# Kernel tuning notes

Hardware: AMD Instinct MI355X
Metric: run time of the kernel (lower is better)

The kernel has to match this reference:

```python
import jax, jax.numpy as jnp
import numpy as np

EMBED_DIM = 1024
NUM_HEADS = 16
HEAD_DIM = EMBED_DIM // NUM_HEADS
B, NQ, K = 2, 2048, 2048


def setup_inputs() -> dict:
    key = jax.random.key(0)
    ks = jax.random.split(key, 11)
    s = 1.0 / np.sqrt(EMBED_DIM)
    return {
        "Q_input": jax.random.normal(ks[0], (B, NQ, EMBED_DIM), jnp.float32),
        "K_input": jax.random.normal(ks[1], (B, K, EMBED_DIM), jnp.float32),
        "V_input": jax.random.normal(ks[2], (B, K, EMBED_DIM), jnp.float32),
        "Wq": jax.random.normal(ks[3], (EMBED_DIM, EMBED_DIM), jnp.float32) * s,
        "bq": jnp.zeros((EMBED_DIM,), jnp.float32),
        "Wk": jax.random.normal(ks[4], (EMBED_DIM, EMBED_DIM), jnp.float32) * s,
        "bk": jnp.zeros((EMBED_DIM,), jnp.float32),
        "Wv": jax.random.normal(ks[5], (EMBED_DIM, EMBED_DIM), jnp.float32) * s,
        "bv": jnp.zeros((EMBED_DIM,), jnp.float32),
        "Wo": jax.random.normal(ks[6], (EMBED_DIM, EMBED_DIM), jnp.float32) * s,
        "bo": jnp.zeros((EMBED_DIM,), jnp.float32),
    }


def reference(Q_input, K_input, V_input, Wq, bq, Wk, bk, Wv, bv, Wo, bo):
    b, n_q, _ = Q_input.shape
    k = K_input.shape[1]
    # Linear projections (torch Linear: x @ W.T + b)
    Q = Q_input @ Wq.T + bq
    Kp = K_input @ Wk.T + bk
    V = V_input @ Wv.T + bv
    # [b, h, s, d]
    Q = Q.reshape(b, n_q, NUM_HEADS, HEAD_DIM).transpose(0, 2, 1, 3)
    Kp = Kp.reshape(b, k, NUM_HEADS, HEAD_DIM).transpose(0, 2, 1, 3)
    V = V.reshape(b, k, NUM_HEADS, HEAD_DIM).transpose(0, 2, 1, 3)
    scores = jnp.einsum("bhqd,bhkd->bhqk", Q, Kp) / jnp.sqrt(jnp.float32(HEAD_DIM))
    weights = jax.nn.softmax(scores, axis=-1)
    attn = jnp.einsum("bhqk,bhkd->bhqd", weights, V)
    attn = attn.transpose(0, 2, 1, 3).reshape(b, n_q, EMBED_DIM)
    return attn @ Wo.T + bo
```

## Files before the change

kernel.cpp:

```cpp
#include <hip/hip_runtime.h>
#include <hip/hip_bf16.h>

typedef __bf16  bf16x8 __attribute__((ext_vector_type(8)));
typedef float   f32x4  __attribute__((ext_vector_type(4)));

#define EMB   1024
#define QSTR  3072
#define HD    64
#define NH    16
#define SEQ   2048
#define BATCH 2
#define TOKENS (BATCH*SEQ)
#define TK    64

typedef __attribute__((address_space(1))) unsigned int* gp_t;
typedef __attribute__((address_space(3))) unsigned int* lp_t;
__device__ __forceinline__ void gload16(const __bf16* g, __bf16* l) {
    __builtin_amdgcn_global_load_lds((gp_t)(unsigned long long)(const void*)g,
                                     (lp_t)(unsigned int)(unsigned long long)(void*)l,
                                     16, 0, 0);
}

__global__ __launch_bounds__(256) void cvt4_kernel(
    const float* __restrict__ s0, const float* __restrict__ s1,
    const float* __restrict__ s2, const float* __restrict__ s3,
    __bf16* __restrict__ dst, int n_per)
{
    const float* s = (blockIdx.y == 0) ? s0 : (blockIdx.y == 1) ? s1
                   : (blockIdx.y == 2) ? s2 : s3;
    int i = (blockIdx.x * 256 + threadIdx.x) * 8;
    if (i >= n_per) return;
    float4 a = *(const float4*)(s + i);
    float4 b = *(const float4*)(s + i + 4);
    __bf16 o[8] = {(__bf16)a.x, (__bf16)a.y, (__bf16)a.z, (__bf16)a.w,
                   (__bf16)b.x, (__bf16)b.y, (__bf16)b.z, (__bf16)b.w};
    *(uint4*)(dst + (size_t)blockIdx.y * n_per + i) = *(const uint4*)o;
}

template <typename TY>
__global__ __launch_bounds__(256) void gemm_fast(
    const __bf16* __restrict__ X, const __bf16* __restrict__ Wt,
    const float* __restrict__ b0, const float* __restrict__ b1,
    const float* __restrict__ b2, TY* __restrict__ Y, int ldy)
{
    __shared__ __align__(16) __bf16 As[2][128 * 64];
    __shared__ __align__(16) __bf16 Bs[2][64 * 64];

    const int tid  = threadIdx.x;
    const int wave = tid >> 6;
    const int lane = tid & 63;
    const int quad = lane >> 4;
    const int l16  = lane & 15;
    const int warp_m = wave >> 1;
    const int warp_n = wave & 1;

    const int bm = blockIdx.y;
    const int bn = blockIdx.x;

    const int lr = lane >> 3;
    const int lc = (lane & 7) ^ lr;
    const __bf16* Ag = X + (size_t)(bn >> 4) * TOKENS * EMB
                         + (size_t)(bm * 128 + wave * 32 + lr) * EMB + lc * 8;
    const __bf16* Bg = Wt + (size_t)(bn * 64 + wave * 16 + lr) * EMB + lc * 8;
    const int aoff = wave * 2048;
    const int boff = wave * 1024;

    f32x4 acc[4][2] = {};

    gload16(Ag,            As[0] + aoff);
    gload16(Ag +  8 * EMB, As[0] + aoff + 512);
    gload16(Ag + 16 * EMB, As[0] + aoff + 1024);
    gload16(Ag + 24 * EMB, As[0] + aoff + 1536);
    gload16(Bg,            Bs[0] + boff);
    gload16(Bg +  8 * EMB, Bs[0] + boff + 512);

    for (int t = 0; t < EMB / 64; ++t) {
        const int cur = t & 1, nxt = cur ^ 1;
        __syncthreads();
        if (t + 1 < EMB / 64) {
            const __bf16* a0 = Ag + (t + 1) * 64;
            const __bf16* w0 = Bg + (t + 1) * 64;
            gload16(a0,            As[nxt] + aoff);
            gload16(a0 +  8 * EMB, As[nxt] + aoff + 512);
            gload16(a0 + 16 * EMB, As[nxt] + aoff + 1024);
            gload16(a0 + 24 * EMB, As[nxt] + aoff + 1536);
            gload16(w0,            Bs[nxt] + boff);
            gload16(w0 +  8 * EMB, Bs[nxt] + boff + 512);
        }

        #pragma unroll
        for (int kk = 0; kk < 2; ++kk) {
            bf16x8 af[4], bf[2];
            #pragma unroll
            for (int i = 0; i < 4; ++i) {
                int row = warp_m * 64 + i * 16 + l16;
                af[i] = *(const bf16x8*)(As[cur] + (row * 8 + ((kk * 4 + quad) ^ (row & 7))) * 8);
            }
            #pragma unroll
            for (int j = 0; j < 2; ++j) {
                int row = warp_n * 32 + j * 16 + l16;
                bf[j] = *(const bf16x8*)(Bs[cur] + (row * 8 + ((kk * 4 + quad) ^ (row & 7))) * 8);
            }
            #pragma unroll
            for (int i = 0; i < 4; ++i)
                #pragma unroll
                for (int j = 0; j < 2; ++j)
                    acc[i][j] = __builtin_amdgcn_mfma_f32_16x16x32_bf16(af[i], bf[j], acc[i][j], 0, 0, 0);
        }
    }

    #pragma unroll
    for (int i = 0; i < 4; ++i)
        #pragma unroll
        for (int j = 0; j < 2; ++j) {
            int n = bn * 64 + warp_n * 32 + j * 16 + l16;
            const float* bsel = (n < 1024) ? b0 : (n < 2048) ? b1 : b2;
            float bj = bsel[n & 1023];
            #pragma unroll
            for (int r = 0; r < 4; ++r) {
                int m = bm * 128 + warp_m * 64 + i * 16 + quad * 4 + r;
                Y[(size_t)m * ldy + n] = (TY)(acc[i][j][r] + bj);
            }
        }
}

__global__ __launch_bounds__(256) void attn_kernel(
    const __bf16* __restrict__ QKV, __bf16* __restrict__ Op)
{
    __shared__ __bf16 Ks[2][64][72];
    __shared__ __bf16 Vt[2][64][72];
    __shared__ __bf16 Plds[4][16][72];

    const int tid  = threadIdx.x;
    const int wave = tid >> 6;
    const int lane = tid & 63;
    const int quad = lane >> 4;
    const int l16  = lane & 15;

    const int qt = blockIdx.x;
    const int h  = blockIdx.y;
    const int b  = blockIdx.z;

    const size_t qoff  = (size_t)b * SEQ * QSTR + (size_t)h * HD;
    const size_t obase = (size_t)b * SEQ * EMB  + (size_t)h * HD;
    const int qbase = qt * 64 + wave * 16;

    const __bf16* qrow = QKV + qoff + (size_t)(qbase + l16) * QSTR;
    bf16x8 aq0 = *(const bf16x8*)(qrow +      quad * 8);
    bf16x8 aq1 = *(const bf16x8*)(qrow + 32 + quad * 8);
    #pragma unroll
    for (int i = 0; i < 8; ++i) {
        aq0[i] = (__bf16)((float)aq0[i] * 0.125f);
        aq1[i] = (__bf16)((float)aq1[i] * 0.125f);
    }

    float l_run[4] = {0.f, 0.f, 0.f, 0.f};
    f32x4 oacc[4] = {};

    const __bf16* Kg = QKV + qoff + EMB;
    const __bf16* Vg = QKV + qoff + 2 * EMB;

    const int srow = tid >> 3;
    const int scol = (tid & 7) << 3;
    const int g0 = srow >> 3;
    const int g1 = g0 + 4;

    {
        uint4 k0 = *(const uint4*)(Kg + (size_t)(srow     ) * QSTR + scol);
        uint4 k1 = *(const uint4*)(Kg + (size_t)(srow + 32) * QSTR + scol);
        uint4 v0 = *(const uint4*)(Vg + (size_t)(srow     ) * QSTR + scol);
        uint4 v1 = *(const uint4*)(Vg + (size_t)(srow + 32) * QSTR + scol);
        *(uint4*)&Ks[0][srow     ][scol] = k0;
        *(uint4*)&Ks[0][srow + 32][scol] = k1;
        const __bf16* p0 = (const __bf16*)&v0;
        const __bf16* p1 = (const __bf16*)&v1;
        #pragma unroll
        for (int j = 0; j < 8; ++j) {
            int d  = scol + j;
            int gg = (d >> 3) & 7;
            Vt[0][d][((g0 ^ gg) << 3) + (srow & 7)] = p0[j];
            Vt[0][d][((g1 ^ gg) << 3) + (srow & 7)] = p1[j];
        }
    }
    __syncthreads();

    for (int t = 0; t < SEQ / TK; ++t) {
        const int cur = t & 1, nxt = cur ^ 1;
        const bool have_next = (t + 1) < SEQ / TK;
        uint4 nk0, nk1, nv0, nv1;
        if (have_next) {
            int kb = (t + 1) * TK;
            nk0 = *(const uint4*)(Kg + (size_t)(kb + srow     ) * QSTR + scol);
            nk1 = *(const uint4*)(Kg + (size_t)(kb + srow + 32) * QSTR + scol);
            nv0 = *(const uint4*)(Vg + (size_t)(kb + srow     ) * QSTR + scol);
            nv1 = *(const uint4*)(Vg + (size_t)(kb + srow + 32) * QSTR + scol);
        }

        f32x4 s[4] = {};
        #pragma unroll
        for (int kb16 = 0; kb16 < 4; ++kb16) {
            bf16x8 klo = *(const bf16x8*)&Ks[cur][kb16 * 16 + l16][     quad * 8];
            bf16x8 khi = *(const bf16x8*)&Ks[cur][kb16 * 16 + l16][32 + quad * 8];
            s[kb16] = __builtin_amdgcn_mfma_f32_16x16x32_bf16(aq0, klo, s[kb16], 0, 0, 0);
            s[kb16] = __builtin_amdgcn_mfma_f32_16x16x32_bf16(aq1, khi, s[kb16], 0, 0, 0);
        }

        #pragma unroll
        for (int kb16 = 0; kb16 < 4; ++kb16)
            #pragma unroll
            for (int r = 0; r < 4; ++r) {
                float e = __expf(s[kb16][r]);
                s[kb16][r] = e;
                l_run[r] += e;
            }

        #pragma unroll
        for (int kb16 = 0; kb16 < 4; ++kb16)
            #pragma unroll
            for (int r = 0; r < 4; ++r)
                Plds[wave][quad * 4 + r][kb16 * 16 + l16] = (__bf16)s[kb16][r];
        __builtin_amdgcn_fence(__ATOMIC_ACQ_REL, "workgroup");

        bf16x8 ap0 = *(const bf16x8*)&Plds[wave][l16][     quad * 8];
        bf16x8 ap1 = *(const bf16x8*)&Plds[wave][l16][32 + quad * 8];
        #pragma unroll
        for (int dt = 0; dt < 4; ++dt) {
            int d  = dt * 16 + l16;
            int gg = (d >> 3) & 7;
            bf16x8 bv0 = *(const bf16x8*)&Vt[cur][d][(( quad     ^ gg) << 3)];
            bf16x8 bv1 = *(const bf16x8*)&Vt[cur][d][(((quad + 4) ^ gg) << 3)];
            oacc[dt] = __builtin_amdgcn_mfma_f32_16x16x32_bf16(ap0, bv0, oacc[dt], 0, 0, 0);
            oacc[dt] = __builtin_amdgcn_mfma_f32_16x16x32_bf16(ap1, bv1, oacc[dt], 0, 0, 0);
        }

        if (have_next) {
            *(uint4*)&Ks[nxt][srow     ][scol] = nk0;
            *(uint4*)&Ks[nxt][srow + 32][scol] = nk1;
            const __bf16* p0 = (const __bf16*)&nv0;
            const __bf16* p1 = (const __bf16*)&nv1;
            #pragma unroll
            for (int j = 0; j < 8; ++j) {
                int d  = scol + j;
                int gg = (d >> 3) & 7;
                Vt[nxt][d][((g0 ^ gg) << 3) + (srow & 7)] = p0[j];
                Vt[nxt][d][((g1 ^ gg) << 3) + (srow & 7)] = p1[j];
            }
        }
        __syncthreads();
    }

    #pragma unroll
    for (int off = 1; off < 16; off <<= 1)
        #pragma unroll
        for (int r = 0; r < 4; ++r)
            l_run[r] += __shfl_xor(l_run[r], off, 64);

    #pragma unroll
    for (int dt = 0; dt < 4; ++dt)
        #pragma unroll
        for (int r = 0; r < 4; ++r) {
            int q = qbase + quad * 4 + r;
            float v = oacc[dt][r] / l_run[r];
            Op[obase + (size_t)q * EMB + dt * 16 + l16] = (__bf16)v;
        }
}

extern "C" void kernel_launch(void* const* d_in, const int* in_sizes, int n_in,
                              void* d_out, int out_size, void* d_ws, size_t ws_size,
                              hipStream_t stream) {
    const float* Qin = (const float*)d_in[0];
    const float* Kin = (const float*)d_in[1];
    const float* Vin = (const float*)d_in[2];
    const float* Wq  = (const float*)d_in[3];
    const float* bq  = (const float*)d_in[4];
    const float* Wk  = (const float*)d_in[5];
    const float* bk  = (const float*)d_in[6];
    const float* Wv  = (const float*)d_in[7];
    const float* bv  = (const float*)d_in[8];
    const float* Wo  = (const float*)d_in[9];
    const float* bo  = (const float*)d_in[10];

    const size_t TENS = (size_t)TOKENS * EMB;
    const size_t WEL  = (size_t)EMB * EMB;
    __bf16* ws = (__bf16*)d_ws;
    __bf16* Xin  = ws;
    __bf16* Wb   = ws + 3 * TENS;
    __bf16* QKVp = ws + 3 * TENS + 4 * WEL;
    __bf16* Ap   = ws;

    cvt4_kernel<<<dim3((unsigned)(TENS / 2048), 3), 256, 0, stream>>>(
        Qin, Kin, Vin, Vin, Xin, (int)TENS);
    cvt4_kernel<<<dim3((unsigned)(WEL / 2048), 4), 256, 0, stream>>>(
        Wq, Wk, Wv, Wo, Wb, (int)WEL);

    gemm_fast<__bf16><<<dim3(QSTR / 64, TOKENS / 128), 256, 0, stream>>>(
        Xin, Wb, bq, bk, bv, QKVp, QSTR);

    attn_kernel<<<dim3(SEQ / 64, NH, BATCH), 256, 0, stream>>>(QKVp, Ap);

    gemm_fast<float><<<dim3(EMB / 64, TOKENS / 128), 256, 0, stream>>>(
        Ap, Wb + 3 * WEL, bo, bo, bo, (float*)d_out, EMB);
}
```

Baseline: 252.9 us.

## Use 128x128 QKV GEMM tiles and process 32 queries per wave in attention

Adds a dedicated QKV projection GEMM with 128x128 output tiles and a K-step of 32, each wave computing a 64x64 sub-tile with a new swizzle and a launch bound of 3 blocks per SM. The attention kernel now handles 128 queries per block, so each wave covers two 16-row query groups and reuses every K/V tile loaded into shared memory for twice as many queries. Together these raise arithmetic intensity and cut global and LDS traffic per FLOP. The cost is more accumulator registers, possibly lower occupancy, and half as many attention blocks, which could hurt load balance.

```diff
diff --git a/kernel.cpp b/kernel.cpp
--- a/kernel.cpp
+++ b/kernel.cpp
@@ -37,14 +37,13 @@
     *(uint4*)(dst + (size_t)blockIdx.y * n_per + i) = *(const uint4*)o;
 }
 
-template <typename TY>
-__global__ __launch_bounds__(256) void gemm_fast(
+__global__ __launch_bounds__(256, 3) void gemm_qkv(
     const __bf16* __restrict__ X, const __bf16* __restrict__ Wt,
     const float* __restrict__ b0, const float* __restrict__ b1,
-    const float* __restrict__ b2, TY* __restrict__ Y, int ldy)
+    const float* __restrict__ b2, __bf16* __restrict__ Y)
 {
-    __shared__ __align__(16) __bf16 As[2][128 * 64];
-    __shared__ __align__(16) __bf16 Bs[2][64 * 64];
+    __shared__ __align__(16) __bf16 As[2][128 * 32];
+    __shared__ __align__(16) __bf16 Bs[2][128 * 32];
 
     const int tid  = threadIdx.x;
     const int wave = tid >> 6;
@@ -57,10 +56,84 @@
     const int bm = blockIdx.y;
     const int bn = blockIdx.x;
 
+    const int lr = lane >> 2;
+    const int lc = (lane & 3) ^ ((lr >> 1) & 3);
+    const __bf16* Ag = X + (size_t)(bn >> 3) * TOKENS * EMB
+                         + (size_t)(bm * 128 + wave * 32 + lr) * EMB + lc * 8;
+    const __bf16* Bg = Wt + (size_t)(bn * 128 + wave * 32 + lr) * EMB + lc * 8;
+    const int off = wave * 1024;
+
+    f32x4 acc[4][4] = {};
+
+    gload16(Ag,            As[0] + off);
+    gload16(Ag + 16 * EMB, As[0] + off + 512);
+    gload16(Bg,            Bs[0] + off);
+    gload16(Bg + 16 * EMB, Bs[0] + off + 512);
+
+    for (int t = 0; t < EMB / 32; ++t) {
+        const int cur = t & 1, nxt = cur ^ 1;
+        __syncthreads();
+        if (t + 1 < EMB / 32) {
+            const __bf16* a0 = Ag + (t + 1) * 32;
+            const __bf16* w0 = Bg + (t + 1) * 32;
+            gload16(a0,            As[nxt] + off);
+            gload16(a0 + 16 * EMB, As[nxt] + off + 512);
+            gload16(w0,            Bs[nxt] + off);
+            gload16(w0 + 16 * EMB, Bs[nxt] + off + 512);
+        }
+
+        bf16x8 af[4], bf[4];
+        #pragma unroll
+        for (int i = 0; i < 4; ++i) {
+            int rowa = warp_m * 64 + i * 16 + l16;
+            int rowb = warp_n * 64 + i * 16 + l16;
+            af[i] = *(const bf16x8*)(As[cur] + (rowa * 4 + (quad ^ ((rowa >> 1) & 3))) * 8);
+            bf[i] = *(const bf16x8*)(Bs[cur] + (rowb * 4 + (quad ^ ((rowb >> 1) & 3))) * 8);
+        }
+        #pragma unroll
+        for (int i = 0; i < 4; ++i)
+            #pragma unroll
+            for (int j = 0; j < 4; ++j)
+                acc[i][j] = __builtin_amdgcn_mfma_f32_16x16x32_bf16(af[i], bf[j], acc[i][j], 0, 0, 0);
+    }
+
+    #pragma unroll
+    for (int i = 0; i < 4; ++i)
+        #pragma unroll
+        for (int j = 0; j < 4; ++j) {
+            int n = bn * 128 + warp_n * 64 + j * 16 + l16;
+            const float* bsel = (n < 1024) ? b0 : (n < 2048) ? b1 : b2;
+            float bj = bsel[n & 1023];
+            #pragma unroll
+            for (int r = 0; r < 4; ++r) {
+                int m = bm * 128 + warp_m * 64 + i * 16 + quad * 4 + r;
+                Y[(size_t)m * QSTR + n] = (__bf16)(acc[i][j][r] + bj);
+            }
+        }
+}
+
+template <typename TY>
+__global__ __launch_bounds__(256) void gemm_fast(
+    const __bf16* __restrict__ X, const __bf16* __restrict__ Wt,
+    const float* __restrict__ b0, TY* __restrict__ Y, int ldy)
+{
+    __shared__ __align__(16) __bf16 As[2][128 * 64];
+    __shared__ __align__(16) __bf16 Bs[2][64 * 64];
+
+    const int tid  = threadIdx.x;
+    const int wave = tid >> 6;
+    const int lane = tid & 63;
+    const int quad = lane >> 4;
+    const int l16  = lane & 15;
+    const int warp_m = wave >> 1;
+    const int warp_n = wave & 1;
+
+    const int bm = blockIdx.y;
+    const int bn = blockIdx.x;
+
     const int lr = lane >> 3;
     const int lc = (lane & 7) ^ lr;
-    const __bf16* Ag = X + (size_t)(bn >> 4) * TOKENS * EMB
-                         + (size_t)(bm * 128 + wave * 32 + lr) * EMB + lc * 8;
+    const __bf16* Ag = X + (size_t)(bm * 128 + wave * 32 + lr) * EMB + lc * 8;
     const __bf16* Bg = Wt + (size_t)(bn * 64 + wave * 16 + lr) * EMB + lc * 8;
     const int aoff = wave * 2048;
     const int boff = wave * 1024;
@@ -114,8 +187,7 @@
         #pragma unroll
         for (int j = 0; j < 2; ++j) {
             int n = bn * 64 + warp_n * 32 + j * 16 + l16;
-            const float* bsel = (n < 1024) ? b0 : (n < 2048) ? b1 : b2;
-            float bj = bsel[n & 1023];
+            float bj = b0[n];
             #pragma unroll
             for (int r = 0; r < 4; ++r) {
                 int m = bm * 128 + warp_m * 64 + i * 16 + quad * 4 + r;
@@ -129,7 +201,7 @@
 {
     __shared__ __bf16 Ks[2][64][72];
     __shared__ __bf16 Vt[2][64][72];
-    __shared__ __bf16 Plds[4][16][72];
+    __shared__ __bf16 Plds[4][32][72];
 
     const int tid  = threadIdx.x;
     const int wave = tid >> 6;
@@ -143,19 +215,23 @@
 
     const size_t qoff  = (size_t)b * SEQ * QSTR + (size_t)h * HD;
     const size_t obase = (size_t)b * SEQ * EMB  + (size_t)h * HD;
-    const int qbase = qt * 64 + wave * 16;
-
-    const __bf16* qrow = QKV + qoff + (size_t)(qbase + l16) * QSTR;
-    bf16x8 aq0 = *(const bf16x8*)(qrow +      quad * 8);
-    bf16x8 aq1 = *(const bf16x8*)(qrow + 32 + quad * 8);
-    #pragma unroll
-    for (int i = 0; i < 8; ++i) {
-        aq0[i] = (__bf16)((float)aq0[i] * 0.125f);
-        aq1[i] = (__bf16)((float)aq1[i] * 0.125f);
-    }
-
-    float l_run[4] = {0.f, 0.f, 0.f, 0.f};
-    f32x4 oacc[4] = {};
+    const int qbase = qt * 128 + wave * 16;
+
+    bf16x8 aq[2][2];
+    #pragma unroll
+    for (int sub = 0; sub < 2; ++sub) {
+        const __bf16* qrow = QKV + qoff + (size_t)(qbase + sub * 64 + l16) * QSTR;
+        aq[sub][0] = *(const bf16x8*)(qrow +      quad * 8);
+        aq[sub][1] = *(const bf16x8*)(qrow + 32 + quad * 8);
+        #pragma unroll
+        for (int i = 0; i < 8; ++i) {
+            aq[sub][0][i] = (__bf16)((float)aq[sub][0][i] * 0.125f);
+            aq[sub][1][i] = (__bf16)((float)aq[sub][1][i] * 0.125f);
+        }
+    }
+
+    float l_run[2][4] = {};
+    f32x4 oacc[2][4] = {};
 
     const __bf16* Kg = QKV + qoff + EMB;
     const __bf16* Vg = QKV + qoff + 2 * EMB;
@@ -196,41 +272,55 @@
             nv1 = *(const uint4*)(Vg + (size_t)(kb + srow + 32) * QSTR + scol);
         }
 
-        f32x4 s[4] = {};
+        f32x4 s[2][4] = {};
         #pragma unroll
         for (int kb16 = 0; kb16 < 4; ++kb16) {
             bf16x8 klo = *(const bf16x8*)&Ks[cur][kb16 * 16 + l16][     quad * 8];
             bf16x8 khi = *(const bf16x8*)&Ks[cur][kb16 * 16 + l16][32 + quad * 8];
-            s[kb16] = __builtin_amdgcn_mfma_f32_16x16x32_bf16(aq0, klo, s[kb16], 0, 0, 0);
-            s[kb16] = __builtin_amdgcn_mfma_f32_16x16x32_bf16(aq1, khi, s[kb16], 0, 0, 0);
-        }
-
-        #pragma unroll
-        for (int kb16 = 0; kb16 < 4; ++kb16)
-            #pragma unroll
-            for (int r = 0; r < 4; ++r) {
-                float e = __expf(s[kb16][r]);
-                s[kb16][r] = e;
-                l_run[r] += e;
-            }
-
-        #pragma unroll
-        for (int kb16 = 0; kb16 < 4; ++kb16)
-            #pragma unroll
-            for (int r = 0; r < 4; ++r)
-                Plds[wave][quad * 4 + r][kb16 * 16 + l16] = (__bf16)s[kb16][r];
+            #pragma unroll
+            for (int sub = 0; sub < 2; ++sub) {
+                s[sub][kb16] = __builtin_amdgcn_mfma_f32_16x16x32_bf16(aq[sub][0], klo, s[sub][kb16], 0, 0, 0);
+                s[sub][kb16] = __builtin_amdgcn_mfma_f32_16x16x32_bf16(aq[sub][1], khi, s[sub][kb16], 0, 0, 0);
+            }
+        }
+
+        #pragma unroll
+        for (int sub = 0; sub < 2; ++sub)
+            #pragma unroll
+            for (int kb16 = 0; kb16 < 4; ++kb16)
+                #pragma unroll
+                for (int r = 0; r < 4; ++r) {
+                    float e = __expf(s[sub][kb16][r]);
+                    s[sub][kb16][r] = e;
+                    l_run[sub][r] += e;
+                }
+
+        #pragma unroll
+        for (int sub = 0; sub < 2; ++sub)
+            #pragma unroll
+            for (int kb16 = 0; kb16 < 4; ++kb16)
+                #pragma unroll
+                for (int r = 0; r < 4; ++r)
+                    Plds[wave][sub * 16 + quad * 4 + r][kb16 * 16 + l16] = (__bf16)s[sub][kb16][r];
         __builtin_amdgcn_fence(__ATOMIC_ACQ_REL, "workgroup");
 
-        bf16x8 ap0 = *(const bf16x8*)&Plds[wave][l16][     quad * 8];
-        bf16x8 ap1 = *(const bf16x8*)&Plds[wave][l16][32 + quad * 8];
+        bf16x8 ap[2][2];
+        #pragma unroll
+        for (int sub = 0; sub < 2; ++sub) {
+            ap[sub][0] = *(const bf16x8*)&Plds[wave][sub * 16 + l16][     quad * 8];
+            ap[sub][1] = *(const bf16x8*)&Plds[wave][sub * 16 + l16][32 + quad * 8];
+        }
         #pragma unroll
         for (int dt = 0; dt < 4; ++dt) {
             int d  = dt * 16 + l16;
             int gg = (d >> 3) & 7;
             bf16x8 bv0 = *(const bf16x8*)&Vt[cur][d][(( quad     ^ gg) << 3)];
             bf16x8 bv1 = *(const bf16x8*)&Vt[cur][d][(((quad + 4) ^ gg) << 3)];
-            oacc[dt] = __builtin_amdgcn_mfma_f32_16x16x32_bf16(ap0, bv0, oacc[dt], 0, 0, 0);
-            oacc[dt] = __builtin_amdgcn_mfma_f32_16x16x32_bf16(ap1, bv1, oacc[dt], 0, 0, 0);
+            #pragma unroll
+            for (int sub = 0; sub < 2; ++sub) {
+                oacc[sub][dt] = __builtin_amdgcn_mfma_f32_16x16x32_bf16(ap[sub][0], bv0, oacc[sub][dt], 0, 0, 0);
+                oacc[sub][dt] = __builtin_amdgcn_mfma_f32_16x16x32_bf16(ap[sub][1], bv1, oacc[sub][dt], 0, 0, 0);
+            }
         }
 
         if (have_next) {
@@ -252,17 +342,21 @@
     #pragma unroll
     for (int off = 1; off < 16; off <<= 1)
         #pragma unroll
-        for (int r = 0; r < 4; ++r)
-            l_run[r] += __shfl_xor(l_run[r], off, 64);
-
-    #pragma unroll
-    for (int dt = 0; dt < 4; ++dt)
-        #pragma unroll
-        for (int r = 0; r < 4; ++r) {
-            int q = qbase + quad * 4 + r;
-            float v = oacc[dt][r] / l_run[r];
-            Op[obase + (size_t)q * EMB + dt * 16 + l16] = (__bf16)v;
-        }
+        for (int sub = 0; sub < 2; ++sub)
+            #pragma unroll
+            for (int r = 0; r < 4; ++r)
+                l_run[sub][r] += __shfl_xor(l_run[sub][r], off, 64);
+
+    #pragma unroll
+    for (int sub = 0; sub < 2; ++sub)
+        #pragma unroll
+        for (int dt = 0; dt < 4; ++dt)
+            #pragma unroll
+            for (int r = 0; r < 4; ++r) {
+                int q = qbase + sub * 64 + quad * 4 + r;
+                float v = oacc[sub][dt][r] / l_run[sub][r];
+                Op[obase + (size_t)q * EMB + dt * 16 + l16] = (__bf16)v;
+            }
 }
 
 extern "C" void kernel_launch(void* const* d_in, const int* in_sizes, int n_in,
@@ -293,11 +387,11 @@
     cvt4_kernel<<<dim3((unsigned)(WEL / 2048), 4), 256, 0, stream>>>(
         Wq, Wk, Wv, Wo, Wb, (int)WEL);
 
-    gemm_fast<__bf16><<<dim3(QSTR / 64, TOKENS / 128), 256, 0, stream>>>(
-        Xin, Wb, bq, bk, bv, QKVp, QSTR);
-
-    attn_kernel<<<dim3(SEQ / 64, NH, BATCH), 256, 0, stream>>>(QKVp, Ap);
+    gemm_qkv<<<dim3(QSTR / 128, TOKENS / 128), 256, 0, stream>>>(
+        Xin, Wb, bq, bk, bv, QKVp);
+
+    attn_kernel<<<dim3(SEQ / 128, NH, BATCH), 256, 0, stream>>>(QKVp, Ap);
 
     gemm_fast<float><<<dim3(EMB / 64, TOKENS / 128), 256, 0, stream>>>(
-        Ap, Wb + 3 * WEL, bo, bo, bo, (float*)d_out, EMB);
-}
+        Ap, Wb + 3 * WEL, bo, (float*)d_out, EMB);
+}
```

After: 239.5 us. 1.06x faster.
